# Performance work log

Measured on AMD Instinct MI355X. Metric: run time of the kernel, lower is better.

## Reference

```python
import jax, jax.numpy as jnp
import numpy as np

B, T, D, H, F = 4, 2048, 1024, 16, 4096
HD = D // H
EPS = 1e-5


def setup_inputs() -> dict:
    key = jax.random.key(0)
    ks = jax.random.split(key, 10)
    s = lambda fan_in: 1.0 / np.sqrt(fan_in)
    return {
        "x": jax.random.normal(ks[0], (B, T, D), jnp.float32),
        "ln1_g": jnp.ones((D,), jnp.float32),
        "ln1_b": jnp.zeros((D,), jnp.float32),
        "ln2_g": jnp.ones((D,), jnp.float32),
        "ln2_b": jnp.zeros((D,), jnp.float32),
        "Wq": jax.random.normal(ks[1], (H, D, HD), jnp.float32) * s(D),
        "Wk": jax.random.normal(ks[2], (H, D, HD), jnp.float32) * s(D),
        "Wv": jax.random.normal(ks[3], (H, D, HD), jnp.float32) * s(D),
        "Wo": jax.random.normal(ks[4], (D, D), jnp.float32) * s(D),
        "bo": jnp.zeros((D,), jnp.float32),
        "W1": jax.random.normal(ks[5], (D, F), jnp.float32) * s(D),
        "b1": jnp.zeros((F,), jnp.float32),
        "W2": jax.random.normal(ks[6], (F, D), jnp.float32) * s(F),
        "b2": jnp.zeros((D,), jnp.float32),
    }


def _layernorm(x, g, b):
    mu = jnp.mean(x, axis=-1, keepdims=True)
    var = jnp.mean(jnp.square(x - mu), axis=-1, keepdims=True)
    return (x - mu) * jax.lax.rsqrt(var + EPS) * g + b


def reference(x, ln1_g, ln1_b, ln2_g, ln2_b, Wq, Wk, Wv, Wo, bo, W1, b1, W2, b2):
    Bc, Tc, Dc = x.shape
    xn = _layernorm(x, ln1_g, ln1_b)
    # per-head projections (source loops over heads; here batched over h)
    q = jnp.einsum('btd,hdk->bhtk', xn, Wq)
    k = jnp.einsum('btd,hdk->bhtk', xn, Wk)
    v = jnp.einsum('btd,hdk->bhtk', xn, Wv)
    scale = jnp.asarray(Dc, x.dtype) ** -0.5  # C**-0.5 with C = embedding_dim
    scores = jnp.einsum('bhtk,bhsk->bhts', q, k) * scale
    causal = jnp.tril(jnp.ones((Tc, Tc), bool))
    scores = jnp.where(causal, scores, -jnp.inf)
    attn = jax.nn.softmax(scores, axis=-1)
    out = jnp.einsum('bhts,bhsk->bhtk', attn, v)
    out = out.transpose(0, 2, 1, 3).reshape(Bc, Tc, Dc)  # concat heads
    attn_out = out @ Wo + bo
    h = attn_out + x  # residual 1
    hn = _layernorm(h, ln2_g, ln2_b)
    ff = jax.nn.relu(hn @ W1 + b1) @ W2 + b2
    return ff + h  # residual 2
```

## Files before the change

kernel.cpp:

```cpp
#include <hip/hip_runtime.h>
#include <hip/hip_bf16.h>

#define NB 4
#define NT 2048
#define ND 1024
#define NH 16
#define NHD 64
#define NF 4096
#define MTOK (NB*NT)

typedef float f32x4 __attribute__((ext_vector_type(4)));
typedef __bf16 bf16x8 __attribute__((ext_vector_type(8)));
typedef short s16x8 __attribute__((ext_vector_type(8)));
typedef short s16x4v __attribute__((ext_vector_type(4)));
typedef unsigned short ushort_t;

__device__ inline ushort_t f2bf(float f) {
    unsigned int u = __builtin_bit_cast(unsigned int, f);
    unsigned int r = (u + 0x7FFFu + ((u >> 16) & 1u)) >> 16;
    return (ushort_t)r;
}

__device__ __forceinline__ void async_load16(const void* g, void* l) {
    __builtin_amdgcn_global_load_lds(
        (const __attribute__((address_space(1))) void*)g,
        (__attribute__((address_space(3))) void*)l, 16, 0, 0);
}

__device__ __forceinline__ unsigned int cvt_pk_bf16(float lo, float hi) {
    unsigned int r;
    asm("v_cvt_pk_bf16_f32 %0, %1, %2" : "=v"(r) : "v"(lo), "v"(hi));
    return r;
}

__global__ __launch_bounds__(256)
void transpose_to_bf16(const float* __restrict__ src, ushort_t* __restrict__ dst,
                       int R, int C) {
    __shared__ float tile[32][33];
    int c0 = blockIdx.x * 32, r0 = blockIdx.y * 32;
    #pragma unroll
    for (int i = 0; i < 32; i += 8)
        tile[threadIdx.y + i][threadIdx.x] =
            src[(size_t)(r0 + threadIdx.y + i) * C + c0 + threadIdx.x];
    __syncthreads();
    #pragma unroll
    for (int i = 0; i < 32; i += 8)
        dst[(size_t)(c0 + threadIdx.y + i) * R + r0 + threadIdx.x] =
            f2bf(tile[threadIdx.x][threadIdx.y + i]);
}

__global__ __launch_bounds__(256)
void transpose_qkv_to_bf16(const float* __restrict__ Wq, const float* __restrict__ Wk,
                           const float* __restrict__ Wv, ushort_t* __restrict__ dst) {
    __shared__ float tile[32][33];
    int z = blockIdx.z;
    int w = z >> 4, h = z & 15;
    const float* src = (w == 0 ? Wq : (w == 1 ? Wk : Wv)) + (size_t)h * ND * NHD;
    const float sc = (w == 0) ? 0.03125f : 1.0f;
    ushort_t* out = dst + ((size_t)w * ND + h * NHD) * ND;
    int c0 = blockIdx.x * 32, r0 = blockIdx.y * 32;
    #pragma unroll
    for (int i = 0; i < 32; i += 8)
        tile[threadIdx.y + i][threadIdx.x] =
            src[(size_t)(r0 + threadIdx.y + i) * NHD + c0 + threadIdx.x];
    __syncthreads();
    #pragma unroll
    for (int i = 0; i < 32; i += 8)
        out[(size_t)(c0 + threadIdx.y + i) * ND + r0 + threadIdx.x] =
            f2bf(tile[threadIdx.x][threadIdx.y + i] * sc);
}

__global__ __launch_bounds__(256)
void layernorm_to_bf16(const float* __restrict__ x, const float* __restrict__ g,
                       const float* __restrict__ bvec, ushort_t* __restrict__ out) {
    int row = blockIdx.x;
    const float4* xr = (const float4*)(x + (size_t)row * ND);
    float4 v = xr[threadIdx.x];
    float s = v.x + v.y + v.z + v.w;
    float s2 = v.x * v.x + v.y * v.y + v.z * v.z + v.w * v.w;
    #pragma unroll
    for (int o = 32; o >= 1; o >>= 1) {
        s += __shfl_xor(s, o);
        s2 += __shfl_xor(s2, o);
    }
    __shared__ float red[8];
    int wave = threadIdx.x >> 6, lane = threadIdx.x & 63;
    if (lane == 0) { red[wave] = s; red[4 + wave] = s2; }
    __syncthreads();
    float ts = red[0] + red[1] + red[2] + red[3];
    float ts2 = red[4] + red[5] + red[6] + red[7];
    float mu = ts * (1.f / ND);
    float var = ts2 * (1.f / ND) - mu * mu;
    float rs = rsqrtf(var + 1e-5f);
    float4 gv = ((const float4*)g)[threadIdx.x];
    float4 bv = ((const float4*)bvec)[threadIdx.x];
    ushort4 o4;
    o4.x = f2bf((v.x - mu) * rs * gv.x + bv.x);
    o4.y = f2bf((v.y - mu) * rs * gv.y + bv.y);
    o4.z = f2bf((v.z - mu) * rs * gv.z + bv.z);
    o4.w = f2bf((v.w - mu) * rs * gv.w + bv.w);
    ((ushort4*)(out + (size_t)row * ND))[threadIdx.x] = o4;
}

template<bool HAS_BIAS, bool RELU, bool HAS_RES, bool OUT_F32>
__global__ __launch_bounds__(256)
void gemm_bf16(const ushort_t* __restrict__ A, const ushort_t* __restrict__ Bt,
               const float* __restrict__ bias, const float* __restrict__ res,
               void* __restrict__ outp, int M, int N, int K) {
    __shared__ __align__(16) ushort_t As[128 * 64];
    __shared__ __align__(16) ushort_t Bs[128 * 64];
    const int t = threadIdx.x;
    const int wave = t >> 6, lane = t & 63;
    const int m0 = blockIdx.y * 128, n0 = blockIdx.x * 128;
    const int wr = (wave >> 1) * 64, wc = (wave & 1) * 64;
    const int rw = lane >> 3;
    const int ck = lane & 7;
    const int srcCol = (ck ^ rw) * 8;
    f32x4 acc[4][4] = {};

    const ushort_t* Abase = A + (size_t)m0 * K + srcCol;
    const ushort_t* Bbase = Bt + (size_t)n0 * K + srcCol;

    for (int kt = 0; kt < K; kt += 64) {
        __syncthreads();
        #pragma unroll
        for (int c = 0; c < 4; c++) {
            const int rowbase = c * 32 + wave * 8;
            const size_t goff = (size_t)(rowbase + rw) * K + kt;
            async_load16(Abase + goff, As + rowbase * 64);
            async_load16(Bbase + goff, Bs + rowbase * 64);
        }
        __syncthreads();
        #pragma unroll
        for (int ks = 0; ks < 2; ks++) {
            bf16x8 af[4], bfr[4];
            #pragma unroll
            for (int m = 0; m < 4; m++) {
                int row = wr + m * 16 + (lane & 15);
                int a = row * 128 + (ks * 32 + 8 * (lane >> 4)) * 2;
                a ^= ((row & 7) << 4);
                af[m] = *(const bf16x8*)((const char*)As + a);
            }
            #pragma unroll
            for (int n = 0; n < 4; n++) {
                int row = wc + n * 16 + (lane & 15);
                int a = row * 128 + (ks * 32 + 8 * (lane >> 4)) * 2;
                a ^= ((row & 7) << 4);
                bfr[n] = *(const bf16x8*)((const char*)Bs + a);
            }
            #pragma unroll
            for (int m = 0; m < 4; m++)
                #pragma unroll
                for (int n = 0; n < 4; n++)
                    acc[m][n] = __builtin_amdgcn_mfma_f32_16x16x32_bf16(
                        af[m], bfr[n], acc[m][n], 0, 0, 0);
        }
    }

    const int gr0 = m0 + wr + (lane >> 4) * 4;
    const int gc0 = n0 + wc + (lane & 15);
    #pragma unroll
    for (int mf = 0; mf < 4; mf++) {
        #pragma unroll
        for (int nf = 0; nf < 4; nf++) {
            int col = gc0 + nf * 16;
            float bb = 0.f;
            if constexpr (HAS_BIAS) bb = bias[col];
            #pragma unroll
            for (int r = 0; r < 4; r++) {
                int row = gr0 + mf * 16 + r;
                float v = acc[mf][nf][r] + bb;
                if constexpr (RELU) v = fmaxf(v, 0.f);
                if constexpr (HAS_RES) v += res[(size_t)row * N + col];
                if constexpr (OUT_F32)
                    ((float*)outp)[(size_t)row * N + col] = v;
                else
                    ((ushort_t*)outp)[(size_t)row * N + col] = f2bf(v);
            }
        }
    }
}

__global__ __launch_bounds__(512)
void attn_kernel(const ushort_t* __restrict__ qkv, ushort_t* __restrict__ out) {
    __shared__ __align__(16) ushort_t Ks[64][72];
    __shared__ __align__(16) ushort_t Vt[64 * 64];
    __shared__ unsigned int Pw[8][16][35];
    const int pairIdx = blockIdx.x, bh = blockIdx.y;
    const int b = bh >> 4, h = bh & 15;
    const int t = threadIdx.x, wave = t >> 6, lane = t & 63;
    const int g = lane >> 4, q16 = lane & 15;
    const size_t base = ((size_t)b * NT) * 3072 + h * NHD;
    const ushort_t* qb = qkv + base;
    const ushort_t* kb = qkv + base + 1024;
    const ushort_t* vb = qkv + base + 2048;
    const int krow = t >> 3, kcol = (t & 7) * 8;
    const int vkp = t >> 4, vdg = t & 15;
    unsigned int* pr = &Pw[wave][q16][0];

    for (int half = 0; half < 2; half++) {
        const int qt = half ? (15 - pairIdx) : pairIdx;
        const int q0 = qt * 128;
        const int wq0 = q0 + wave * 16;
        const int wq = wq0 + q16;
        bf16x8 qf[2];
        {
            const ushort_t* qp = qb + (size_t)wq * 3072 + 8 * g;
            qf[0] = *(const bf16x8*)qp;
            qf[1] = *(const bf16x8*)(qp + 32);
        }
        f32x4 of[4] = {};
        float m_run = -1.0e30f, l_run = 0.f;
        const int nkv = 2 * qt + 2;

        for (int kv = 0; kv < nkv; ++kv) {
            __syncthreads();
            *(bf16x8*)&Ks[krow][kcol] =
                *(const bf16x8*)(kb + (size_t)(kv * 64 + krow) * 3072 + kcol);
            {
                const ushort_t* vp = vb + (size_t)(kv * 64 + 2 * vkp) * 3072 + vdg * 4;
                s16x4v v0 = *(const s16x4v*)vp;
                s16x4v v1 = *(const s16x4v*)(vp + 3072);
                #pragma unroll
                for (int dd = 0; dd < 4; dd++) {
                    int d = vdg * 4 + dd;
                    unsigned int wv = (unsigned int)(ushort_t)v0[dd] |
                                      ((unsigned int)(ushort_t)v1[dd] << 16);
                    int a = (d << 7) + (vkp << 2);
                    a ^= (((d & 7) ^ ((d >> 3) & 7)) << 4);
                    *(unsigned int*)((char*)Vt + a) = wv;
                }
            }
            __syncthreads();

            const int kbase = kv * 64;
            if (kbase > wq0 + 15) continue;

            f32x4 sf[4] = {};
            #pragma unroll
            for (int n = 0; n < 4; n++) {
                #pragma unroll
                for (int kd = 0; kd < 2; kd++) {
                    bf16x8 kf = *(const bf16x8*)&Ks[n * 16 + q16][kd * 32 + 8 * g];
                    sf[n] = __builtin_amdgcn_mfma_f32_16x16x32_bf16(kf, qf[kd], sf[n], 0, 0, 0);
                }
            }

            const bool partial = (kbase + 63 > wq0);
            float p[4][4];
            #pragma unroll
            for (int n = 0; n < 4; n++)
                #pragma unroll
                for (int r = 0; r < 4; r++) {
                    float v = sf[n][r];
                    if (partial) {
                        int kg = kbase + n * 16 + 4 * g + r;
                        if (kg > wq) v = -1.0e30f;
                    }
                    p[n][r] = v;
                }

            float mx0 = fmaxf(fmaxf(p[0][0], p[0][1]), fmaxf(p[0][2], p[0][3]));
            float mx1 = fmaxf(fmaxf(p[1][0], p[1][1]), fmaxf(p[1][2], p[1][3]));
            float mx2 = fmaxf(fmaxf(p[2][0], p[2][1]), fmaxf(p[2][2], p[2][3]));
            float mx3 = fmaxf(fmaxf(p[3][0], p[3][1]), fmaxf(p[3][2], p[3][3]));
            float mx = fmaxf(fmaxf(mx0, mx1), fmaxf(mx2, mx3));
            mx = fmaxf(mx, __shfl_xor(mx, 16));
            mx = fmaxf(mx, __shfl_xor(mx, 32));

            if (__any(mx > m_run + 8.f)) {
                float mn = fmaxf(m_run, mx);
                float corr = __expf(m_run - mn);
                m_run = mn;
                l_run *= corr;
                #pragma unroll
                for (int nf = 0; nf < 4; nf++) {
                    f32x4 o4 = of[nf];
                    o4[0] *= corr; o4[1] *= corr; o4[2] *= corr; o4[3] *= corr;
                    of[nf] = o4;
                }
            }

            float ps = 0.f;
            #pragma unroll
            for (int n = 0; n < 4; n++)
                #pragma unroll
                for (int r = 0; r < 4; r++) {
                    p[n][r] = __expf(p[n][r] - m_run);
                    ps += p[n][r];
                }
            ps += __shfl_xor(ps, 16);
            ps += __shfl_xor(ps, 32);
            l_run += ps;

            #pragma unroll
            for (int n = 0; n < 4; n++) {
                pr[8 * n + 2 * g + 0] = cvt_pk_bf16(p[n][0], p[n][1]);
                pr[8 * n + 2 * g + 1] = cvt_pk_bf16(p[n][2], p[n][3]);
            }
            #pragma unroll
            for (int kbk = 0; kbk < 2; kbk++) {
                uint4 pu;
                pu.x = pr[16 * kbk + 4 * g + 0];
                pu.y = pr[16 * kbk + 4 * g + 1];
                pu.z = pr[16 * kbk + 4 * g + 2];
                pu.w = pr[16 * kbk + 4 * g + 3];
                bf16x8 pf = __builtin_bit_cast(bf16x8, pu);
                #pragma unroll
                for (int nf = 0; nf < 4; nf++) {
                    const int d = nf * 16 + q16;
                    int a = (d << 7) + (kbk * 64 + 16 * g);
                    a ^= (((d & 7) ^ ((d >> 3) & 7)) << 4);
                    bf16x8 vf = *(const bf16x8*)((const char*)Vt + a);
                    of[nf] = __builtin_amdgcn_mfma_f32_16x16x32_bf16(
                        vf, pf, of[nf], 0, 0, 0);
                }
            }
        }

        float rl = 1.f / l_run;
        const size_t orow = (size_t)b * NT + q0 + wave * 16 + q16;
        #pragma unroll
        for (int nf = 0; nf < 4; nf++) {
            ushort4 o4;
            o4.x = f2bf(of[nf][0] * rl);
            o4.y = f2bf(of[nf][1] * rl);
            o4.z = f2bf(of[nf][2] * rl);
            o4.w = f2bf(of[nf][3] * rl);
            *(ushort4*)(out + orow * ND + h * NHD + nf * 16 + 4 * g) = o4;
        }
    }
}

extern "C" void kernel_launch(void* const* d_in, const int* in_sizes, int n_in,
                              void* d_out, int out_size, void* d_ws, size_t ws_size,
                              hipStream_t stream) {
    const float* x     = (const float*)d_in[0];
    const float* ln1_g = (const float*)d_in[1];
    const float* ln1_b = (const float*)d_in[2];
    const float* ln2_g = (const float*)d_in[3];
    const float* ln2_b = (const float*)d_in[4];
    const float* Wq    = (const float*)d_in[5];
    const float* Wk    = (const float*)d_in[6];
    const float* Wv    = (const float*)d_in[7];
    const float* Wo    = (const float*)d_in[8];
    const float* bo    = (const float*)d_in[9];
    const float* W1    = (const float*)d_in[10];
    const float* b1    = (const float*)d_in[11];
    const float* W2    = (const float*)d_in[12];
    const float* b2    = (const float*)d_in[13];
    float* outp = (float*)d_out;

    char* w = (char*)d_ws;
    ushort_t* Wqkv_t = (ushort_t*)(w);
    ushort_t* Wo_t   = (ushort_t*)(w + 6291456);
    ushort_t* W1_t   = (ushort_t*)(w + 8388608);
    ushort_t* W2_t   = (ushort_t*)(w + 16777216);
    ushort_t* xn     = (ushort_t*)(w + 25165824);
    ushort_t* qkv    = (ushort_t*)(w + 41943040);
    ushort_t* attn_o = qkv + (size_t)MTOK * 3072;
    ushort_t* ff1    = qkv;
    float*    hbuf   = (float*)(w + 41943040 + 67108864);

    dim3 tb(32, 8);
    transpose_qkv_to_bf16<<<dim3(2, 32, 48), tb, 0, stream>>>(Wq, Wk, Wv, Wqkv_t);
    transpose_to_bf16<<<dim3(32, 32), tb, 0, stream>>>(Wo, Wo_t, 1024, 1024);
    transpose_to_bf16<<<dim3(128, 32), tb, 0, stream>>>(W1, W1_t, 1024, 4096);
    transpose_to_bf16<<<dim3(32, 128), tb, 0, stream>>>(W2, W2_t, 4096, 1024);

    layernorm_to_bf16<<<MTOK, 256, 0, stream>>>(x, ln1_g, ln1_b, xn);

    gemm_bf16<false, false, false, false><<<dim3(24, 64), 256, 0, stream>>>(
        xn, Wqkv_t, nullptr, nullptr, qkv, MTOK, 3072, 1024);

    attn_kernel<<<dim3(8, 64), 512, 0, stream>>>(qkv, attn_o);

    gemm_bf16<true, false, true, true><<<dim3(8, 64), 256, 0, stream>>>(
        attn_o, Wo_t, bo, x, hbuf, MTOK, 1024, 1024);

    layernorm_to_bf16<<<MTOK, 256, 0, stream>>>(hbuf, ln2_g, ln2_b, xn);

    gemm_bf16<true, true, false, false><<<dim3(32, 64), 256, 0, stream>>>(
        xn, W1_t, b1, nullptr, ff1, MTOK, NF, 1024);

    gemm_bf16<true, false, true, true><<<dim3(8, 64), 256, 0, stream>>>(
        ff1, W2_t, b2, hbuf, outp, MTOK, 1024, NF);
}
```

Before: 408.0 us.

## Enlarge attention query tiles, use exp2 softmax, async K loads, XCD-aware block remap

The attention kernel now gives each wave 32 query rows instead of 16, so each K and V tile in LDS is reused across twice as many queries. K is loaded with async global-to-LDS copies into a swizzled layout. Softmax uses a raw v_exp_f32 with log2(e) folded into the Q weight scale, and the rescale threshold moves from 8 to 11.5. The GEMM and attention kernels also remap block indices so neighbouring tiles share an XCD for better L2 locality. In exchange, the attention grid halves to 256 blocks, which may underfill the GPU and worsen load balance, and register pressure rises.

Result: no change. 400.4 us (-1.9%).

```diff
diff --git a/kernel.cpp b/kernel.cpp
--- a/kernel.cpp
+++ b/kernel.cpp
@@ -33,6 +33,12 @@
     return r;
 }
 
+__device__ __forceinline__ float exp2_fast(float x) {
+    float r;
+    asm("v_exp_f32 %0, %1" : "=v"(r) : "v"(x));
+    return r;
+}
+
 __global__ __launch_bounds__(256)
 void transpose_to_bf16(const float* __restrict__ src, ushort_t* __restrict__ dst,
                        int R, int C) {
@@ -56,7 +62,7 @@
     int z = blockIdx.z;
     int w = z >> 4, h = z & 15;
     const float* src = (w == 0 ? Wq : (w == 1 ? Wk : Wv)) + (size_t)h * ND * NHD;
-    const float sc = (w == 0) ? 0.03125f : 1.0f;
+    const float sc = (w == 0) ? 0.03125f * 1.44269504f : 1.0f;
     ushort_t* out = dst + ((size_t)w * ND + h * NHD) * ND;
     int c0 = blockIdx.x * 32, r0 = blockIdx.y * 32;
     #pragma unroll
@@ -111,7 +117,10 @@
     __shared__ __align__(16) ushort_t Bs[128 * 64];
     const int t = threadIdx.x;
     const int wave = t >> 6, lane = t & 63;
-    const int m0 = blockIdx.y * 128, n0 = blockIdx.x * 128;
+    int wid = blockIdx.y * gridDim.x + blockIdx.x;
+    const int cpx = (gridDim.x * gridDim.y) >> 3;
+    wid = (wid & 7) * cpx + (wid >> 3);
+    const int m0 = (wid / gridDim.x) * 128, n0 = (wid % gridDim.x) * 128;
     const int wr = (wave >> 1) * 64, wc = (wave & 1) * 64;
     const int rw = lane >> 3;
     const int ck = lane & 7;
@@ -183,40 +192,44 @@
 
 __global__ __launch_bounds__(512)
 void attn_kernel(const ushort_t* __restrict__ qkv, ushort_t* __restrict__ out) {
-    __shared__ __align__(16) ushort_t Ks[64][72];
+    __shared__ __align__(16) ushort_t Ks[64 * 64];
     __shared__ __align__(16) ushort_t Vt[64 * 64];
-    __shared__ unsigned int Pw[8][16][35];
-    const int pairIdx = blockIdx.x, bh = blockIdx.y;
+    __shared__ unsigned int Pw[8][32][35];
+    const int L = blockIdx.y * gridDim.x + blockIdx.x;
+    const int xcd = L & 7, kk = L >> 3;
+    const int bh = ((kk & 7) << 3) | xcd;
+    const int pairIdx = kk >> 3;
     const int b = bh >> 4, h = bh & 15;
     const int t = threadIdx.x, wave = t >> 6, lane = t & 63;
     const int g = lane >> 4, q16 = lane & 15;
     const size_t base = ((size_t)b * NT) * 3072 + h * NHD;
-    const ushort_t* qb = qkv + base;
+    const ushort_t* qp_base = qkv + base;
     const ushort_t* kb = qkv + base + 1024;
     const ushort_t* vb = qkv + base + 2048;
-    const int krow = t >> 3, kcol = (t & 7) * 8;
+    const int krw = lane >> 3, kck = lane & 7;
+    ushort_t* klds = Ks + wave * 8 * 64;
+    const int ksrc = (kck ^ krw) * 8;
     const int vkp = t >> 4, vdg = t & 15;
-    unsigned int* pr = &Pw[wave][q16][0];
 
     for (int half = 0; half < 2; half++) {
-        const int qt = half ? (15 - pairIdx) : pairIdx;
-        const int q0 = qt * 128;
-        const int wq0 = q0 + wave * 16;
-        const int wq = wq0 + q16;
-        bf16x8 qf[2];
-        {
-            const ushort_t* qp = qb + (size_t)wq * 3072 + 8 * g;
-            qf[0] = *(const bf16x8*)qp;
-            qf[1] = *(const bf16x8*)(qp + 32);
-        }
-        f32x4 of[4] = {};
-        float m_run = -1.0e30f, l_run = 0.f;
-        const int nkv = 2 * qt + 2;
+        const int qt = half ? (7 - pairIdx) : pairIdx;
+        const int q0 = qt * 256;
+        const int wq0 = q0 + wave * 32;
+        bf16x8 qf[2][2];
+        #pragma unroll
+        for (int qb2 = 0; qb2 < 2; qb2++) {
+            const ushort_t* qp = qp_base + (size_t)(wq0 + 16 * qb2 + q16) * 3072 + 8 * g;
+            qf[qb2][0] = *(const bf16x8*)qp;
+            qf[qb2][1] = *(const bf16x8*)(qp + 32);
+        }
+        f32x4 of[2][4] = {};
+        float m_run[2] = {-1.0e30f, -1.0e30f};
+        float l_run[2] = {0.f, 0.f};
+        const int nkv = 4 * qt + 4;
 
         for (int kv = 0; kv < nkv; ++kv) {
             __syncthreads();
-            *(bf16x8*)&Ks[krow][kcol] =
-                *(const bf16x8*)(kb + (size_t)(kv * 64 + krow) * 3072 + kcol);
+            async_load16(kb + (size_t)(kv * 64 + wave * 8 + krw) * 3072 + ksrc, klds);
             {
                 const ushort_t* vp = vb + (size_t)(kv * 64 + 2 * vkp) * 3072 + vdg * 4;
                 s16x4v v0 = *(const s16x4v*)vp;
@@ -234,100 +247,124 @@
             __syncthreads();
 
             const int kbase = kv * 64;
-            if (kbase > wq0 + 15) continue;
-
-            f32x4 sf[4] = {};
-            #pragma unroll
-            for (int n = 0; n < 4; n++) {
+            if (kbase > wq0 + 31) continue;
+
+            bf16x8 kf[4][2];
+            #pragma unroll
+            for (int n = 0; n < 4; n++)
                 #pragma unroll
                 for (int kd = 0; kd < 2; kd++) {
-                    bf16x8 kf = *(const bf16x8*)&Ks[n * 16 + q16][kd * 32 + 8 * g];
-                    sf[n] = __builtin_amdgcn_mfma_f32_16x16x32_bf16(kf, qf[kd], sf[n], 0, 0, 0);
-                }
-            }
-
-            const bool partial = (kbase + 63 > wq0);
-            float p[4][4];
+                    int row = n * 16 + q16;
+                    int a = row * 128 + (kd * 64 + 16 * g);
+                    a ^= ((row & 7) << 4);
+                    kf[n][kd] = *(const bf16x8*)((const char*)Ks + a);
+                }
+
+            f32x4 sf[2][4] = {};
             #pragma unroll
             for (int n = 0; n < 4; n++)
                 #pragma unroll
-                for (int r = 0; r < 4; r++) {
-                    float v = sf[n][r];
-                    if (partial) {
-                        int kg = kbase + n * 16 + 4 * g + r;
-                        if (kg > wq) v = -1.0e30f;
+                for (int kd = 0; kd < 2; kd++) {
+                    sf[0][n] = __builtin_amdgcn_mfma_f32_16x16x32_bf16(
+                        kf[n][kd], qf[0][kd], sf[0][n], 0, 0, 0);
+                    sf[1][n] = __builtin_amdgcn_mfma_f32_16x16x32_bf16(
+                        kf[n][kd], qf[1][kd], sf[1][n], 0, 0, 0);
+                }
+
+            #pragma unroll
+            for (int qb2 = 0; qb2 < 2; qb2++) {
+                const int wqb = wq0 + 16 * qb2 + q16;
+                const bool partial = (kbase + 63 > wq0 + 16 * qb2);
+                float p[4][4];
+                #pragma unroll
+                for (int n = 0; n < 4; n++)
+                    #pragma unroll
+                    for (int r = 0; r < 4; r++) {
+                        float v = sf[qb2][n][r];
+                        if (partial) {
+                            int kg = kbase + n * 16 + 4 * g + r;
+                            if (kg > wqb) v = -1.0e30f;
+                        }
+                        p[n][r] = v;
                     }
-                    p[n][r] = v;
-                }
-
-            float mx0 = fmaxf(fmaxf(p[0][0], p[0][1]), fmaxf(p[0][2], p[0][3]));
-            float mx1 = fmaxf(fmaxf(p[1][0], p[1][1]), fmaxf(p[1][2], p[1][3]));
-            float mx2 = fmaxf(fmaxf(p[2][0], p[2][1]), fmaxf(p[2][2], p[2][3]));
-            float mx3 = fmaxf(fmaxf(p[3][0], p[3][1]), fmaxf(p[3][2], p[3][3]));
-            float mx = fmaxf(fmaxf(mx0, mx1), fmaxf(mx2, mx3));
-            mx = fmaxf(mx, __shfl_xor(mx, 16));
-            mx = fmaxf(mx, __shfl_xor(mx, 32));
-
-            if (__any(mx > m_run + 8.f)) {
-                float mn = fmaxf(m_run, mx);
-                float corr = __expf(m_run - mn);
-                m_run = mn;
-                l_run *= corr;
-                #pragma unroll
-                for (int nf = 0; nf < 4; nf++) {
-                    f32x4 o4 = of[nf];
-                    o4[0] *= corr; o4[1] *= corr; o4[2] *= corr; o4[3] *= corr;
-                    of[nf] = o4;
-                }
-            }
-
-            float ps = 0.f;
-            #pragma unroll
-            for (int n = 0; n < 4; n++)
-                #pragma unroll
-                for (int r = 0; r < 4; r++) {
-                    p[n][r] = __expf(p[n][r] - m_run);
-                    ps += p[n][r];
-                }
-            ps += __shfl_xor(ps, 16);
-            ps += __shfl_xor(ps, 32);
-            l_run += ps;
-
-            #pragma unroll
-            for (int n = 0; n < 4; n++) {
-                pr[8 * n + 2 * g + 0] = cvt_pk_bf16(p[n][0], p[n][1]);
-                pr[8 * n + 2 * g + 1] = cvt_pk_bf16(p[n][2], p[n][3]);
-            }
+                float mx0 = fmaxf(fmaxf(p[0][0], p[0][1]), fmaxf(p[0][2], p[0][3]));
+                float mx1 = fmaxf(fmaxf(p[1][0], p[1][1]), fmaxf(p[1][2], p[1][3]));
+                float mx2 = fmaxf(fmaxf(p[2][0], p[2][1]), fmaxf(p[2][2], p[2][3]));
+                float mx3 = fmaxf(fmaxf(p[3][0], p[3][1]), fmaxf(p[3][2], p[3][3]));
+                float mx = fmaxf(fmaxf(mx0, mx1), fmaxf(mx2, mx3));
+                mx = fmaxf(mx, __shfl_xor(mx, 16));
+                mx = fmaxf(mx, __shfl_xor(mx, 32));
+                if (__any(mx > m_run[qb2] + 11.5f)) {
+                    float mn = fmaxf(m_run[qb2], mx);
+                    float corr = exp2_fast(m_run[qb2] - mn);
+                    m_run[qb2] = mn;
+                    l_run[qb2] *= corr;
+                    #pragma unroll
+                    for (int nf = 0; nf < 4; nf++) {
+                        f32x4 o4 = of[qb2][nf];
+                        o4[0] *= corr; o4[1] *= corr; o4[2] *= corr; o4[3] *= corr;
+                        of[qb2][nf] = o4;
+                    }
+                }
+                float ps = 0.f;
+                #pragma unroll
+                for (int n = 0; n < 4; n++)
+                    #pragma unroll
+                    for (int r = 0; r < 4; r++) {
+                        p[n][r] = exp2_fast(p[n][r] - m_run[qb2]);
+                        ps += p[n][r];
+                    }
+                ps += __shfl_xor(ps, 16);
+                ps += __shfl_xor(ps, 32);
+                l_run[qb2] += ps;
+                unsigned int* pr = &Pw[wave][16 * qb2 + q16][0];
+                #pragma unroll
+                for (int n = 0; n < 4; n++) {
+                    pr[8 * n + 2 * g + 0] = cvt_pk_bf16(p[n][0], p[n][1]);
+                    pr[8 * n + 2 * g + 1] = cvt_pk_bf16(p[n][2], p[n][3]);
+                }
+            }
+
             #pragma unroll
             for (int kbk = 0; kbk < 2; kbk++) {
-                uint4 pu;
-                pu.x = pr[16 * kbk + 4 * g + 0];
-                pu.y = pr[16 * kbk + 4 * g + 1];
-                pu.z = pr[16 * kbk + 4 * g + 2];
-                pu.w = pr[16 * kbk + 4 * g + 3];
-                bf16x8 pf = __builtin_bit_cast(bf16x8, pu);
+                bf16x8 pfr[2];
+                #pragma unroll
+                for (int qb2 = 0; qb2 < 2; qb2++) {
+                    const unsigned int* pr = &Pw[wave][16 * qb2 + q16][0];
+                    uint4 pu;
+                    pu.x = pr[16 * kbk + 4 * g + 0];
+                    pu.y = pr[16 * kbk + 4 * g + 1];
+                    pu.z = pr[16 * kbk + 4 * g + 2];
+                    pu.w = pr[16 * kbk + 4 * g + 3];
+                    pfr[qb2] = __builtin_bit_cast(bf16x8, pu);
+                }
                 #pragma unroll
                 for (int nf = 0; nf < 4; nf++) {
                     const int d = nf * 16 + q16;
                     int a = (d << 7) + (kbk * 64 + 16 * g);
                     a ^= (((d & 7) ^ ((d >> 3) & 7)) << 4);
                     bf16x8 vf = *(const bf16x8*)((const char*)Vt + a);
-                    of[nf] = __builtin_amdgcn_mfma_f32_16x16x32_bf16(
-                        vf, pf, of[nf], 0, 0, 0);
-                }
-            }
-        }
-
-        float rl = 1.f / l_run;
-        const size_t orow = (size_t)b * NT + q0 + wave * 16 + q16;
+                    of[0][nf] = __builtin_amdgcn_mfma_f32_16x16x32_bf16(
+                        vf, pfr[0], of[0][nf], 0, 0, 0);
+                    of[1][nf] = __builtin_amdgcn_mfma_f32_16x16x32_bf16(
+                        vf, pfr[1], of[1][nf], 0, 0, 0);
+                }
+            }
+        }
+
         #pragma unroll
-        for (int nf = 0; nf < 4; nf++) {
-            ushort4 o4;
-            o4.x = f2bf(of[nf][0] * rl);
-            o4.y = f2bf(of[nf][1] * rl);
-            o4.z = f2bf(of[nf][2] * rl);
-            o4.w = f2bf(of[nf][3] * rl);
-            *(ushort4*)(out + orow * ND + h * NHD + nf * 16 + 4 * g) = o4;
+        for (int qb2 = 0; qb2 < 2; qb2++) {
+            float rl = 1.f / l_run[qb2];
+            const size_t orow = (size_t)b * NT + q0 + wave * 32 + 16 * qb2 + q16;
+            #pragma unroll
+            for (int nf = 0; nf < 4; nf++) {
+                ushort4 o4;
+                o4.x = f2bf(of[qb2][nf][0] * rl);
+                o4.y = f2bf(of[qb2][nf][1] * rl);
+                o4.z = f2bf(of[qb2][nf][2] * rl);
+                o4.w = f2bf(of[qb2][nf][3] * rl);
+                *(ushort4*)(out + orow * ND + h * NHD + nf * 16 + 4 * g) = o4;
+            }
         }
     }
 }
@@ -373,7 +410,7 @@
     gemm_bf16<false, false, false, false><<<dim3(24, 64), 256, 0, stream>>>(
         xn, Wqkv_t, nullptr, nullptr, qkv, MTOK, 3072, 1024);
 
-    attn_kernel<<<dim3(8, 64), 512, 0, stream>>>(qkv, attn_o);
+    attn_kernel<<<dim3(4, 64), 512, 0, stream>>>(qkv, attn_o);
 
     gemm_bf16<true, false, true, true><<<dim3(8, 64), 256, 0, stream>>>(
         attn_o, Wo_t, bo, x, hbuf, MTOK, 1024, 1024);
```
